# Kernel optimization log

Hardware: AMD Instinct MI355X
Metric: run time of the kernel (lower is better)

Reference implementation:

```python
import jax, jax.numpy as jnp
import numpy as np
import math

H = 12          # num_attention_heads
DIM = 768       # hidden_size
HD = DIM // H   # attention_head_size
B = 8           # batch
S = 1024        # max_seqlen
NNZ = B * S     # total_nnz (all sequences full length)


def setup_inputs() -> dict:
    key = jax.random.key(0)
    k1, k2, k3, k4 = jax.random.split(key, 4)
    hidden_states = jax.random.normal(k1, (NNZ, DIM), jnp.float32)
    cu_seqlens = jnp.arange(B + 1, dtype=jnp.int32) * S
    indices = jnp.arange(NNZ, dtype=jnp.int32)
    attn_mask = jnp.ones((B, S), jnp.int32)
    bias = jax.random.normal(k2, (B, H, S, S), jnp.float32) * 0.1
    slopes = jax.random.uniform(k3, (H,), jnp.float32)
    # Wqkv = nn.Linear(DIM, 3*DIM): weight (3*DIM, DIM), bias (3*DIM,)
    Wqkv_w = jax.random.normal(k4, (3 * DIM, DIM), jnp.float32) * (1.0 / math.sqrt(DIM))
    Wqkv_b = jnp.zeros((3 * DIM,), jnp.float32)
    return {
        "hidden_states": hidden_states,
        "cu_seqlens": cu_seqlens,
        "max_seqlen": S,
        "indices": indices,
        "attn_mask": attn_mask,
        "bias": bias,
        "slopes": slopes,
        "Wqkv_w": Wqkv_w,
        "Wqkv_b": Wqkv_b,
    }


def reference(hidden_states, cu_seqlens, max_seqlen, indices, attn_mask, bias, slopes, Wqkv_w, Wqkv_b):
    nnz, dim = hidden_states.shape
    batch = cu_seqlens.shape[0] - 1
    hd = dim // H
    # fused QKV projection on unpadded tokens
    qkv = hidden_states @ Wqkv_w.T + Wqkv_b                      # (nnz, 3*dim)
    # pad_input: scatter tokens into dense (batch*seqlen, 3*dim)
    padded = jnp.zeros((batch * max_seqlen, 3 * dim), qkv.dtype).at[indices].set(qkv)
    qkv = padded.reshape(batch, max_seqlen, 3, H, hd)            # (b, s, 3, h, d)
    q, k, v = qkv[:, :, 0], qkv[:, :, 1], qkv[:, :, 2]           # (b, s, h, d)
    scores = jnp.einsum('bqhd,bkhd->bhqk', q, k) / math.sqrt(hd) + bias
    probs = jax.nn.softmax(scores, axis=-1)                      # (b, h, q, k)
    attn = jnp.einsum('bhqk,bkhd->bqhd', probs, v)               # (b, s, h, d)
    # unpad_input_only: gather valid tokens (attn_mask selects same positions as indices)
    flat = attn.reshape(batch * max_seqlen, dim)
    return flat[indices].reshape(nnz, dim)
```

## Files before the change

kernel.cpp:

```cpp
#include <hip/hip_runtime.h>

#define H_      12
#define DIM_    768
#define HD_     64
#define BATCH_  8
#define SEQ_    1024
#define NNZ_    8192
#define N3_     2304

typedef short sh8 __attribute__((ext_vector_type(8)));
typedef float f32x4 __attribute__((ext_vector_type(4)));

__device__ __forceinline__ unsigned short f2bf(float f) {
    unsigned u = __float_as_uint(f);
    u += 0x7fff + ((u >> 16) & 1);
    return (unsigned short)(u >> 16);
}

__device__ __forceinline__ void glds16(const unsigned short* g, unsigned short* l) {
    __builtin_amdgcn_global_load_lds(
        (const __attribute__((address_space(1))) unsigned int*)g,
        (__attribute__((address_space(3))) unsigned int*)l, 16, 0, 0);
}

__global__ void prep(const float* __restrict__ hidden,
                     const float* __restrict__ W,
                     const int* __restrict__ indices,
                     unsigned short* __restrict__ Xbf,
                     unsigned short* __restrict__ Wbf,
                     int* __restrict__ inv) {
    const int XN4 = NNZ_ * DIM_ / 4;
    const int WN4 = N3_ * DIM_ / 4;
    int i = blockIdx.x * blockDim.x + threadIdx.x;
    if (i < XN4) {
        float4 f = ((const float4*)hidden)[i];
        ushort4 u;
        u.x = f2bf(f.x); u.y = f2bf(f.y); u.z = f2bf(f.z); u.w = f2bf(f.w);
        ((ushort4*)Xbf)[i] = u;
    } else if (i < XN4 + WN4) {
        int k = i - XN4;
        float4 f = ((const float4*)W)[k];
        ushort4 u;
        u.x = f2bf(f.x); u.y = f2bf(f.y); u.z = f2bf(f.z); u.w = f2bf(f.w);
        ((ushort4*)Wbf)[k] = u;
    }
    if (i < NNZ_) inv[indices[i]] = i;
}

#define BK 32
__launch_bounds__(256)
__global__ void qkv_gemm(const unsigned short* __restrict__ X,
                         const unsigned short* __restrict__ W,
                         const float* __restrict__ bqkv,
                         const int* __restrict__ indices,
                         unsigned short* __restrict__ qkvbf) {
    __shared__ __align__(16) unsigned short As[128 * BK];
    __shared__ __align__(16) unsigned short Bs[128 * BK];

    const int bm = blockIdx.x * 128;
    const int bn = blockIdx.y * 128;
    const int t = threadIdx.x;
    const int wave = t >> 6;
    const int lane = t & 63;
    const int l16 = lane & 15;
    const int quad = lane >> 4;
    const int wm = (wave & 1) * 64;
    const int wn = (wave >> 1) * 64;

    f32x4 acc[4][4];
    for (int i = 0; i < 4; i++)
        for (int j = 0; j < 4; j++)
            for (int r = 0; r < 4; r++) acc[i][j][r] = 0.f;

    const int c0 = wave * 2;
    const int r0 = c0 * 16 + (lane >> 2);
    const int colA = (lane & 3) * 8;
    const unsigned short* gA0 = &X[(size_t)(bm + r0) * DIM_ + colA];
    const unsigned short* gA1 = &X[(size_t)(bm + r0 + 16) * DIM_ + colA];
    const unsigned short* gB0 = &W[(size_t)(bn + r0) * DIM_ + colA];
    const unsigned short* gB1 = &W[(size_t)(bn + r0 + 16) * DIM_ + colA];
    unsigned short* lA0 = &As[c0 * 512];
    unsigned short* lA1 = &As[c0 * 512 + 512];
    unsigned short* lB0 = &Bs[c0 * 512];
    unsigned short* lB1 = &Bs[c0 * 512 + 512];

    for (int kk = 0; kk < DIM_; kk += BK) {
        __syncthreads();
        glds16(gA0 + kk, lA0);
        glds16(gA1 + kk, lA1);
        glds16(gB0 + kk, lB0);
        glds16(gB1 + kk, lB1);
        __syncthreads();

        sh8 af[4], wf[4];
        for (int i = 0; i < 4; i++)
            af[i] = *(const sh8*)&As[(wm + i * 16 + l16) * BK + quad * 8];
        for (int j = 0; j < 4; j++)
            wf[j] = *(const sh8*)&Bs[(wn + j * 16 + l16) * BK + quad * 8];
        for (int i = 0; i < 4; i++)
            for (int j = 0; j < 4; j++)
                acc[i][j] = __builtin_amdgcn_mfma_f32_16x16x32_bf16(af[i], wf[j], acc[i][j], 0, 0, 0);
    }

    const size_t plane = (size_t)BATCH_ * H_ * SEQ_ * HD_;
    for (int i = 0; i < 4; i++) {
        for (int r = 0; r < 4; r++) {
            int m = bm + wm + i * 16 + quad * 4 + r;
            int pos = indices[m];
            int b = pos >> 10;
            int s = pos & 1023;
            for (int j = 0; j < 4; j++) {
                int n = bn + wn + j * 16 + l16;
                float val = acc[i][j][r] + bqkv[n];
                int which = n / DIM_;
                int nn = n - which * DIM_;
                int hh = nn >> 6;
                int d = nn & 63;
                size_t off;
                if (which == 2)
                    off = 2 * plane + (((size_t)b * H_ + hh) * HD_ + d) * SEQ_ + s;
                else
                    off = (size_t)which * plane + (((size_t)b * H_ + hh) * SEQ_ + s) * HD_ + d;
                qkvbf[off] = f2bf(val);
            }
        }
    }
}

#define LDP 72
__launch_bounds__(256, 3)
__global__ void attn(const unsigned short* __restrict__ qkvbf,
                     const float* __restrict__ bias,
                     const int* __restrict__ inv,
                     float* __restrict__ out) {
    __shared__ __align__(16) unsigned short Kp[2][2][64 * 32];
    __shared__ __align__(16) unsigned short Vp[2][2][64 * 32];
    __shared__ __align__(16) unsigned short Ps[4][16 * LDP];

    const int orig = blockIdx.y * gridDim.x + blockIdx.x;
    const int swz = (orig & 7) * 192 + (orig >> 3);
    const int qt = swz & 15;
    const int bh = swz >> 4;

    const int t = threadIdx.x;
    const int wave = t >> 6;
    const int lane = t & 63;
    const int l16 = lane & 15;
    const int quad = lane >> 4;
    const int qx = quad ^ (l16 & 3);

    const size_t plane = (size_t)BATCH_ * H_ * SEQ_ * HD_;
    const unsigned short* Q  = qkvbf + (size_t)bh * SEQ_ * HD_;
    const unsigned short* K  = Q + plane;
    const unsigned short* Vt = qkvbf + 2 * plane + (size_t)bh * HD_ * SEQ_;

    const int q0 = qt * 64 + wave * 16;

    sh8 aq[2];
    for (int kk2 = 0; kk2 < 2; kk2++)
        aq[kk2] = *(const sh8*)&Q[(size_t)(q0 + l16) * HD_ + kk2 * 32 + quad * 8];

    float lsum = 0.f;
    f32x4 o[4];
    for (int j = 0; j < 4; j++)
        for (int r = 0; r < 4; r++) o[j][r] = 0.f;

    const float scale = 0.125f;
    const float* brow4 = bias + (size_t)bh * SEQ_ * SEQ_ + (size_t)(q0 + l16) * SEQ_ + quad * 4;

    const int lrow = wave * 16 + (lane >> 2);
    const int lslot = (lane & 3) ^ ((lane >> 2) & 3);
    const unsigned short* gK = &K[(size_t)lrow * HD_ + lslot * 8];
    const unsigned short* gV = &Vt[(size_t)lrow * SEQ_ + lslot * 8];
    unsigned short* lK0[2] = { &Kp[0][0][wave * 512], &Kp[0][1][wave * 512] };
    unsigned short* lK1[2] = { &Kp[1][0][wave * 512], &Kp[1][1][wave * 512] };
    unsigned short* lV0[2] = { &Vp[0][0][wave * 512], &Vp[0][1][wave * 512] };
    unsigned short* lV1[2] = { &Vp[1][0][wave * 512], &Vp[1][1][wave * 512] };

    glds16(gK,      lK0[0]);
    glds16(gK + 32, lK0[1]);
    glds16(gV,      lV0[0]);
    glds16(gV + 32, lV0[1]);
    float4 bv4[4];
    for (int j = 0; j < 4; j++)
        bv4[j] = *(const float4*)(brow4 + j * 16);
    __syncthreads();

    for (int kt = 0; kt < 16; kt++) {
        const int cur = kt & 1;

        if (kt < 15) {
            const int k0n = (kt + 1) * 64;
            if (cur == 0) {
                glds16(gK + (size_t)k0n * HD_,      lK1[0]);
                glds16(gK + (size_t)k0n * HD_ + 32, lK1[1]);
                glds16(gV + k0n,      lV1[0]);
                glds16(gV + k0n + 32, lV1[1]);
            } else {
                glds16(gK + (size_t)k0n * HD_,      lK0[0]);
                glds16(gK + (size_t)k0n * HD_ + 32, lK0[1]);
                glds16(gV + k0n,      lV0[0]);
                glds16(gV + k0n + 32, lV0[1]);
            }
        }
        float4 bvn[4];
        {
            const int kb = ((kt + 1) & 15) * 64;
            for (int j = 0; j < 4; j++)
                bvn[j] = *(const float4*)(brow4 + kb + j * 16);
        }
        __builtin_amdgcn_sched_barrier(0);

        f32x4 sc[4];
        for (int j = 0; j < 4; j++)
            for (int r = 0; r < 4; r++) sc[j][r] = 0.f;
        for (int kk2 = 0; kk2 < 2; kk2++)
            for (int j = 0; j < 4; j++) {
                sh8 bk = *(const sh8*)&Kp[cur][kk2][(j * 16 + l16) * 32 + qx * 8];
                sc[j] = __builtin_amdgcn_mfma_f32_16x16x32_bf16(bk, aq[kk2], sc[j], 0, 0, 0);
            }

        for (int j = 0; j < 4; j++) {
            float4 bb = bv4[j];
            float p0 = __expf(sc[j][0] * scale + bb.x);
            float p1 = __expf(sc[j][1] * scale + bb.y);
            float p2 = __expf(sc[j][2] * scale + bb.z);
            float p3 = __expf(sc[j][3] * scale + bb.w);
            lsum += (p0 + p1) + (p2 + p3);
            ushort4 u;
            u.x = f2bf(p0); u.y = f2bf(p1); u.z = f2bf(p2); u.w = f2bf(p3);
            *(ushort4*)&Ps[wave][l16 * LDP + j * 16 + quad * 4] = u;
        }

        for (int kk2 = 0; kk2 < 2; kk2++) {
            sh8 ap = *(const sh8*)&Ps[wave][l16 * LDP + kk2 * 32 + quad * 8];
            for (int j = 0; j < 4; j++) {
                sh8 vvf = *(const sh8*)&Vp[cur][kk2][(j * 16 + l16) * 32 + qx * 8];
                o[j] = __builtin_amdgcn_mfma_f32_16x16x32_bf16(ap, vvf, o[j], 0, 0, 0);
            }
        }

        __syncthreads();
        for (int j = 0; j < 4; j++) bv4[j] = bvn[j];
    }

    float s0 = lsum;
    s0 += __shfl_xor(s0, 16, 64);
    s0 += __shfl_xor(s0, 32, 64);
    float rl[4];
    for (int r = 0; r < 4; r++)
        rl[r] = 1.0f / __shfl(s0, quad * 4 + r, 64);

    const int b = bh / H_;
    const int hh = bh % H_;
    for (int r = 0; r < 4; r++) {
        int srow_q = q0 + quad * 4 + r;
        int pos = b * SEQ_ + srow_q;
        int i_out = inv[pos];
        for (int j = 0; j < 4; j++)
            out[(size_t)i_out * DIM_ + hh * HD_ + j * 16 + l16] = o[j][r] * rl[r];
    }
}

extern "C" void kernel_launch(void* const* d_in, const int* in_sizes, int n_in,
                              void* d_out, int out_size, void* d_ws, size_t ws_size,
                              hipStream_t stream) {
    const float* hidden  = (const float*)d_in[0];
    const int*   indices = (const int*)d_in[3];
    const float* bias    = (const float*)d_in[5];
    const float* Wqkv_w  = (const float*)d_in[7];
    const float* Wqkv_b  = (const float*)d_in[8];
    float* out = (float*)d_out;

    char* ws = (char*)d_ws;
    unsigned short* Xbf   = (unsigned short*)ws;
    unsigned short* Wbf   = (unsigned short*)(ws + 12582912);
    unsigned short* qkvbf = (unsigned short*)(ws + 16121856);
    int* inv              = (int*)(ws + 53870592);

    const int XN4 = NNZ_ * DIM_ / 4;
    const int WN4 = N3_ * DIM_ / 4;
    prep<<<(XN4 + WN4 + 255) / 256, 256, 0, stream>>>(hidden, Wqkv_w, indices, Xbf, Wbf, inv);
    qkv_gemm<<<dim3(NNZ_ / 128, N3_ / 128), 256, 0, stream>>>(Xbf, Wbf, Wqkv_b, indices, qkvbf);
    attn<<<dim3(SEQ_ / 64, BATCH_ * H_), 256, 0, stream>>>(qkvbf, bias, inv, out);
}
```

Baseline: 624.9 us.

## Double-buffer QKV GEMM LDS loads, swizzle tile order, fix LDS bank swizzle

The QKV GEMM now double-buffers its LDS tiles, prefetching the next K-slice with global_load_lds while MFMAs run on the current one. This halves the barriers per iteration. It also remaps block indices so neighbouring blocks share A/B tiles in cache, and XOR-swizzles LDS slots to cut bank conflicts. The attention kernel's swizzle is changed to the same (l16>>1) pattern. LDS use doubles, and the swizzle must stay consistent between the writers and readers.

```diff
diff --git a/kernel.cpp b/kernel.cpp
--- a/kernel.cpp
+++ b/kernel.cpp
@@ -54,11 +54,15 @@
                          const float* __restrict__ bqkv,
                          const int* __restrict__ indices,
                          unsigned short* __restrict__ qkvbf) {
-    __shared__ __align__(16) unsigned short As[128 * BK];
-    __shared__ __align__(16) unsigned short Bs[128 * BK];
-
-    const int bm = blockIdx.x * 128;
-    const int bn = blockIdx.y * 128;
+    __shared__ __align__(16) unsigned short As[2][128 * BK];
+    __shared__ __align__(16) unsigned short Bs[2][128 * BK];
+
+    const int orig = blockIdx.y * gridDim.x + blockIdx.x;
+    const int c = orig & 7;
+    const int local = orig >> 3;
+    const int bm = ((c & 3) * 16 + (local & 15)) * 128;
+    const int bn = ((c >> 2) * 9 + (local >> 4)) * 128;
+
     const int t = threadIdx.x;
     const int wave = t >> 6;
     const int lane = t & 63;
@@ -66,6 +70,7 @@
     const int quad = lane >> 4;
     const int wm = (wave & 1) * 64;
     const int wn = (wave >> 1) * 64;
+    const int qxr = quad ^ ((l16 >> 1) & 3);
 
     f32x4 acc[4][4];
     for (int i = 0; i < 4; i++)
@@ -74,32 +79,49 @@
 
     const int c0 = wave * 2;
     const int r0 = c0 * 16 + (lane >> 2);
-    const int colA = (lane & 3) * 8;
-    const unsigned short* gA0 = &X[(size_t)(bm + r0) * DIM_ + colA];
-    const unsigned short* gA1 = &X[(size_t)(bm + r0 + 16) * DIM_ + colA];
-    const unsigned short* gB0 = &W[(size_t)(bn + r0) * DIM_ + colA];
-    const unsigned short* gB1 = &W[(size_t)(bn + r0 + 16) * DIM_ + colA];
-    unsigned short* lA0 = &As[c0 * 512];
-    unsigned short* lA1 = &As[c0 * 512 + 512];
-    unsigned short* lB0 = &Bs[c0 * 512];
-    unsigned short* lB1 = &Bs[c0 * 512 + 512];
-
-    for (int kk = 0; kk < DIM_; kk += BK) {
-        __syncthreads();
-        glds16(gA0 + kk, lA0);
-        glds16(gA1 + kk, lA1);
-        glds16(gB0 + kk, lB0);
-        glds16(gB1 + kk, lB1);
-        __syncthreads();
+    const int sslot = ((lane & 3) ^ ((lane >> 3) & 3)) * 8;
+    const unsigned short* gA0 = &X[(size_t)(bm + r0) * DIM_ + sslot];
+    const unsigned short* gA1 = &X[(size_t)(bm + r0 + 16) * DIM_ + sslot];
+    const unsigned short* gB0 = &W[(size_t)(bn + r0) * DIM_ + sslot];
+    const unsigned short* gB1 = &W[(size_t)(bn + r0 + 16) * DIM_ + sslot];
+    unsigned short* lA0[2] = { &As[0][c0 * 512], &As[1][c0 * 512] };
+    unsigned short* lB0[2] = { &Bs[0][c0 * 512], &Bs[1][c0 * 512] };
+
+    glds16(gA0, lA0[0]);
+    glds16(gA1, lA0[0] + 512);
+    glds16(gB0, lB0[0]);
+    glds16(gB1, lB0[0] + 512);
+    __syncthreads();
+
+    for (int ks = 0; ks < DIM_ / BK; ks++) {
+        const int cur = ks & 1;
+
+        if (ks < DIM_ / BK - 1) {
+            const int kk = (ks + 1) * BK;
+            if (cur == 0) {
+                glds16(gA0 + kk, lA0[1]);
+                glds16(gA1 + kk, lA0[1] + 512);
+                glds16(gB0 + kk, lB0[1]);
+                glds16(gB1 + kk, lB0[1] + 512);
+            } else {
+                glds16(gA0 + kk, lA0[0]);
+                glds16(gA1 + kk, lA0[0] + 512);
+                glds16(gB0 + kk, lB0[0]);
+                glds16(gB1 + kk, lB0[0] + 512);
+            }
+        }
+        __builtin_amdgcn_sched_barrier(0);
 
         sh8 af[4], wf[4];
         for (int i = 0; i < 4; i++)
-            af[i] = *(const sh8*)&As[(wm + i * 16 + l16) * BK + quad * 8];
+            af[i] = *(const sh8*)&As[cur][(wm + i * 16 + l16) * BK + qxr * 8];
         for (int j = 0; j < 4; j++)
-            wf[j] = *(const sh8*)&Bs[(wn + j * 16 + l16) * BK + quad * 8];
+            wf[j] = *(const sh8*)&Bs[cur][(wn + j * 16 + l16) * BK + qxr * 8];
         for (int i = 0; i < 4; i++)
             for (int j = 0; j < 4; j++)
                 acc[i][j] = __builtin_amdgcn_mfma_f32_16x16x32_bf16(af[i], wf[j], acc[i][j], 0, 0, 0);
+
+        __syncthreads();
     }
 
     const size_t plane = (size_t)BATCH_ * H_ * SEQ_ * HD_;
@@ -147,7 +169,7 @@
     const int lane = t & 63;
     const int l16 = lane & 15;
     const int quad = lane >> 4;
-    const int qx = quad ^ (l16 & 3);
+    const int qx = quad ^ ((l16 >> 1) & 3);
 
     const size_t plane = (size_t)BATCH_ * H_ * SEQ_ * HD_;
     const unsigned short* Q  = qkvbf + (size_t)bh * SEQ_ * HD_;
@@ -169,7 +191,7 @@
     const float* brow4 = bias + (size_t)bh * SEQ_ * SEQ_ + (size_t)(q0 + l16) * SEQ_ + quad * 4;
 
     const int lrow = wave * 16 + (lane >> 2);
-    const int lslot = (lane & 3) ^ ((lane >> 2) & 3);
+    const int lslot = (lane & 3) ^ ((lane >> 3) & 3);
     const unsigned short* gK = &K[(size_t)lrow * HD_ + lslot * 8];
     const unsigned short* gV = &Vt[(size_t)lrow * SEQ_ + lslot * 8];
     unsigned short* lK0[2] = { &Kp[0][0][wave * 512], &Kp[0][1][wave * 512] };
```

New measurement: 625.3 us. No clear change (+0.1%).
